# Kernel optimization log

Measured on AMD Instinct MI355X. Metric: run time of the kernel, lower is better.

## Reference

```python
import jax, jax.numpy as jnp
import numpy as np

B, T, C = 4, 2048, 2048
N_HEAD, N_KV = 16, 4
HD = C // N_HEAD          # 128
N_REP = N_HEAD // N_KV    # 4


def setup_inputs() -> dict:
    key = jax.random.key(0)
    k1, k2, k3 = jax.random.split(key, 3)
    x = jax.random.normal(k1, (B, T, C), dtype=jnp.float32)
    # RoPE frequencies: complex freqs_cis stored as [T, HD//2, 2] = (cos, sin)
    inv_freq = 1.0 / (10000.0 ** (jnp.arange(0, HD, 2, dtype=jnp.float32) / HD))  # [HD//2]
    angles = jnp.arange(T, dtype=jnp.float32)[:, None] * inv_freq[None, :]        # [T, HD//2]
    freqs_cis = jnp.stack([jnp.cos(angles), jnp.sin(angles)], axis=-1)            # [T, HD//2, 2]
    w_qkv = jax.random.normal(k2, (C, (N_HEAD + 2 * N_KV) * HD), dtype=jnp.float32) * 0.02
    w_proj = jax.random.normal(k3, (C, C), dtype=jnp.float32) * 0.02
    return {"x": x, "freqs_cis": freqs_cis, "w_qkv": w_qkv, "w_proj": w_proj}


def _apply_rope(t, freqs_cis):
    # t: [B, T, H, HD]; pairs (even, odd) along last dim form complex numbers
    shp = t.shape
    t2 = t.astype(jnp.float32).reshape(*shp[:-1], HD // 2, 2)
    cos = freqs_cis[None, :, None, :, 0]  # [1, T, 1, HD//2]
    sin = freqs_cis[None, :, None, :, 1]
    re = t2[..., 0] * cos - t2[..., 1] * sin
    im = t2[..., 0] * sin + t2[..., 1] * cos
    return jnp.stack([re, im], axis=-1).reshape(shp).astype(t.dtype)


def reference(x, freqs_cis, w_qkv, w_proj):
    Bs, Ts, Cs = x.shape
    qkv = x @ w_qkv  # [B, T, (H+2KV)*HD]
    q, k, v = jnp.split(qkv, [N_HEAD * HD, N_HEAD * HD + N_KV * HD], axis=-1)
    q = q.reshape(Bs, Ts, N_HEAD, HD)
    k = k.reshape(Bs, Ts, N_KV, HD)
    v = v.reshape(Bs, Ts, N_KV, HD)
    q = _apply_rope(q, freqs_cis)
    k = _apply_rope(k, freqs_cis)
    # GQA attention without materializing repeated k/v: group query heads per kv head
    qg = q.reshape(Bs, Ts, N_KV, N_REP, HD)
    scale = 1.0 / jnp.sqrt(jnp.asarray(HD, dtype=jnp.float32))
    scores = jnp.einsum('btkrd,bskd->bkrts', qg, k) * scale  # [B, KV, REP, T, T]
    att = jax.nn.softmax(scores.astype(jnp.float32), axis=-1).astype(q.dtype)
    y = jnp.einsum('bkrts,bskd->btkrd', att, v).reshape(Bs, Ts, Cs)
    return y @ w_proj
```

## Files before the change

### kernel.cpp

```cpp
#include <hip/hip_runtime.h>

using u16 = unsigned short;
using u32 = unsigned int;
typedef float f32x4 __attribute__((ext_vector_type(4)));
typedef float f32x16 __attribute__((ext_vector_type(16)));
typedef short s16x8 __attribute__((ext_vector_type(8)));
typedef unsigned int u32x4 __attribute__((ext_vector_type(4)));

__device__ __forceinline__ u16 f2bf(float x) {
  u32 u = __float_as_uint(x);
  u += 0x7fffu + ((u >> 16) & 1u);
  return (u16)(u >> 16);
}
__device__ __forceinline__ u32 pack2bf(float lo, float hi) {
  return (u32)f2bf(lo) | ((u32)f2bf(hi) << 16);
}
__device__ __forceinline__ float bf2f(u16 v) {
  return __uint_as_float(((u32)v) << 16);
}
__device__ __forceinline__ u32 cvtpk(float lo, float hi) {
  u32 r;
  asm("v_cvt_pk_bf16_f32 %0, %1, %2" : "=v"(r) : "v"(lo), "v"(hi));
  return r;
}
__device__ __forceinline__ void plswap(u32& a, u32& b) {
  asm volatile("v_permlane32_swap_b32 %0, %1" : "+v"(a), "+v"(b));
}
__device__ __forceinline__ void gload16(const u16* g, u16* l) {
  __builtin_amdgcn_global_load_lds(
      (__attribute__((address_space(1))) void*)(u16*)g,
      (__attribute__((address_space(3))) void*)l, 16, 0, 0);
}
__device__ __forceinline__ f32x4 fzero4() {
  f32x4 v = {0.f, 0.f, 0.f, 0.f};
  return v;
}
__device__ __forceinline__ f32x16 fzero16() {
  f32x16 v = {0, 0, 0, 0, 0, 0, 0, 0, 0, 0, 0, 0, 0, 0, 0, 0};
  return v;
}
__device__ __forceinline__ void barrier_hard() {
  __builtin_amdgcn_sched_barrier(0);
  __builtin_amdgcn_s_barrier();
  __builtin_amdgcn_sched_barrier(0);
}

__global__ __launch_bounds__(256) void k_convert(const float* __restrict__ in,
                                                 u16* __restrict__ out, int n8) {
  int i = blockIdx.x * 256 + threadIdx.x;
  if (i >= n8) return;
  const float4* p = (const float4*)in;
  float4 a = p[2 * i], b = p[2 * i + 1];
  uint4 o;
  o.x = pack2bf(a.x, a.y);
  o.y = pack2bf(a.z, a.w);
  o.z = pack2bf(b.x, b.y);
  o.w = pack2bf(b.z, b.w);
  ((uint4*)out)[i] = o;
}

__global__ __launch_bounds__(256) void k_transpose(const float* __restrict__ w,
                                                   u16* __restrict__ wt, int N, int K) {
  __shared__ float tile[64][65];
  int n0 = blockIdx.x * 64, k0 = blockIdx.y * 64;
  int tid = threadIdx.x;
  int rr = tid >> 6, cc = tid & 63;
#pragma unroll
  for (int p = 0; p < 16; ++p)
    tile[p * 4 + rr][cc] = w[(size_t)(k0 + p * 4 + rr) * N + n0 + cc];
  __syncthreads();
#pragma unroll
  for (int p = 0; p < 16; ++p)
    wt[(size_t)(n0 + p * 4 + rr) * K + k0 + cc] = f2bf(tile[cc][p * 4 + rr]);
}

template <bool OBF>
__global__ __launch_bounds__(512, 2) void k_gemm8(const u16* __restrict__ A,
                                                  const u16* __restrict__ Bt,
                                                  void* __restrict__ Out, int Nd, int Kd) {
  __shared__ u16 Al[2][2][8192];
  __shared__ u16 Bl[2][2][8192];
  u32 bid = blockIdx.x, nwg = gridDim.x;
  u32 wgid = (bid & 7) * (nwg >> 3) + (bid >> 3);
  int ntn = Nd >> 8;
  int bm = wgid / ntn, bn = wgid % ntn;
  int tid = threadIdx.x, w = tid >> 6, lane = tid & 63;
  int wm = w >> 2, wn = w & 3;
  int lq = lane & 15, lg = lane >> 4;

  const u16* Ab = A + (size_t)(bm * 256) * Kd;
  const u16* Bb = Bt + (size_t)(bn * 256) * Kd;

  u32 offA[2][2], offB[2][2];
#pragma unroll
  for (int set = 0; set < 2; ++set)
#pragma unroll
    for (int inst = 0; inst < 2; ++inst) {
      int c = inst * 512 + tid;
      int ldsrow = c >> 4, sl = c & 15;
      int orig = sl ^ (ldsrow & 15);
      int pr = ldsrow * 2 + (orig >> 3);
      int kch = orig & 7;
      int rA = (pr & 63) + ((pr >> 6) & 1) * 128 + set * 64;
      int rB = (pr & 31) + (pr >> 5) * 64 + set * 32;
      offA[set][inst] = (u32)(rA * Kd + kch * 8);
      offB[set][inst] = (u32)(rB * Kd + kch * 8);
    }

  int aoff[4][2], boff[4][2];
#pragma unroll
  for (int mf = 0; mf < 4; ++mf)
#pragma unroll
    for (int kk = 0; kk < 2; ++kk) {
      int pr = wm * 64 + mf * 16 + lq;
      int slot = (((pr & 1) << 3) + kk * 4 + lg) ^ ((pr >> 1) & 15);
      aoff[mf][kk] = (pr >> 1) * 128 + slot * 8;
    }
#pragma unroll
  for (int nf = 0; nf < 4; ++nf)
#pragma unroll
    for (int kk = 0; kk < 2; ++kk) {
      int pr = wn * 32 + (nf & 1) * 16 + lq;
      int slot = (((pr & 1) << 3) + kk * 4 + lg) ^ ((pr >> 1) & 15);
      boff[nf][kk] = (pr >> 1) * 128 + slot * 8;
    }

  int ldsbase = w * 512;

  auto stgA = [&](int dbuf, int set, int u) {
    const u16* s = Ab + u * 64;
    gload16(s + offA[set][0], &Al[dbuf][set][ldsbase]);
    gload16(s + offA[set][1], &Al[dbuf][set][4096 + ldsbase]);
  };
  auto stgB = [&](int dbuf, int set, int u) {
    const u16* s = Bb + u * 64;
    gload16(s + offB[set][0], &Bl[dbuf][set][ldsbase]);
    gload16(s + offB[set][1], &Bl[dbuf][set][4096 + ldsbase]);
  };

  f32x4 acc[8][4];
#pragma unroll
  for (int m = 0; m < 8; ++m)
#pragma unroll
    for (int n = 0; n < 4; ++n) acc[m][n] = fzero4();

  s16x8 af[4][2], bf[4][2];

  auto LDA = [&](int dbuf, int set) {
#pragma unroll
    for (int mf = 0; mf < 4; ++mf)
#pragma unroll
      for (int kk = 0; kk < 2; ++kk)
        af[mf][kk] = *(const s16x8*)&Al[dbuf][set][aoff[mf][kk]];
  };
  auto LDB = [&](int dbuf, int nf0) {
#pragma unroll
    for (int nf = 0; nf < 2; ++nf)
#pragma unroll
      for (int kk = 0; kk < 2; ++kk)
        bf[nf0 + nf][kk] = *(const s16x8*)&Bl[dbuf][nf0 >> 1][boff[nf0 + nf][kk]];
  };
  auto DO_MFMA = [&](int mb, int nb) {
    __builtin_amdgcn_s_setprio(1);
#pragma unroll
    for (int mf = 0; mf < 4; ++mf)
#pragma unroll
      for (int nf = 0; nf < 2; ++nf)
#pragma unroll
        for (int kk = 0; kk < 2; ++kk)
          acc[mb + mf][nb + nf] = __builtin_amdgcn_mfma_f32_16x16x32_bf16(
              af[mf][kk], bf[nb + nf][kk], acc[mb + mf][nb + nf], 0, 0, 0);
    __builtin_amdgcn_s_setprio(0);
  };
  auto LGKM0 = [&]() {
    asm volatile("s_waitcnt lgkmcnt(0)" ::: "memory");
    __builtin_amdgcn_sched_barrier(0);
  };

  int nt = Kd >> 6;
  stgA(0, 0, 0); stgB(0, 0, 0); stgA(0, 1, 0); stgB(0, 1, 0);
  stgA(1, 0, 1); stgB(1, 1, 1); stgA(1, 1, 1);
  asm volatile("s_waitcnt vmcnt(6)" ::: "memory");
  barrier_hard();

  for (int u = 0; u < nt; ++u) {
    int c = u & 1, nc = c ^ 1;
    bool g1 = (u + 1 < nt), g2 = (u + 2 < nt);
    LDA(c, 0);
    LDB(c, 0);
    if (g1) stgB(nc, 0, u + 1);
    barrier_hard();
    LGKM0();
    DO_MFMA(0, 0);
    barrier_hard();
    LDB(c, 2);
    if (g2) stgA(c, 0, u + 2);
    barrier_hard();
    LGKM0();
    DO_MFMA(0, 2);
    barrier_hard();
    LDA(c, 1);
    if (g2) stgB(c, 1, u + 2);
    barrier_hard();
    LGKM0();
    DO_MFMA(4, 2);
    barrier_hard();
    if (g2) stgA(c, 1, u + 2);
    barrier_hard();
    DO_MFMA(4, 0);
    if (g2) {
      asm volatile("s_waitcnt vmcnt(6)" ::: "memory");
    } else {
      asm volatile("s_waitcnt vmcnt(0)" ::: "memory");
    }
    barrier_hard();
  }

  int r0 = bm * 256 + wm * 128, c0 = bn * 256 + wn * 64;
  if (OBF) {
    u16* O = (u16*)Out;
#pragma unroll
    for (int mf = 0; mf < 8; ++mf)
#pragma unroll
      for (int nf = 0; nf < 4; ++nf)
#pragma unroll
        for (int r = 0; r < 4; ++r)
          O[(size_t)(r0 + mf * 16 + lg * 4 + r) * Nd + c0 + nf * 16 + lq] =
              f2bf(acc[mf][nf][r]);
  } else {
    float* O = (float*)Out;
#pragma unroll
    for (int mf = 0; mf < 8; ++mf)
#pragma unroll
      for (int nf = 0; nf < 4; ++nf)
#pragma unroll
        for (int r = 0; r < 4; ++r)
          O[(size_t)(r0 + mf * 16 + lg * 4 + r) * Nd + c0 + nf * 16 + lq] =
              acc[mf][nf][r];
  }
}

__device__ __forceinline__ u32 rope_pair(short a, short b, float c, float s, float sc) {
  float x0 = bf2f((u16)a), x1 = bf2f((u16)b);
  return pack2bf((x0 * c - x1 * s) * sc, (x0 * s + x1 * c) * sc);
}

__global__ __launch_bounds__(256) void k_ropeqk(const u16* __restrict__ qkv,
                                                const float* __restrict__ fr,
                                                u16* __restrict__ Q, u16* __restrict__ K) {
  int idx = blockIdx.x * 256 + threadIdx.x;
  if (idx >= 8192 * 320) return;
  int row = idx / 320, g = idx % 320;
  int b = row >> 11, t = row & 2047;
  int col = g * 8;
  const u16* src = qkv + (size_t)row * 3072 + col;
  int isq = col < 2048;
  float sc = isq ? 0.127517432f : 1.0f;
  int c2 = isq ? col : col - 2048;
  int h = c2 >> 7, d = c2 & 127;
  u16* dst = isq ? (Q + ((size_t)(b * 16 + h) * 2048 + t) * 128 + d)
                 : (K + ((size_t)(b * 4 + h) * 2048 + t) * 128 + d);
  const float4* fp = (const float4*)(fr + (size_t)t * 128 + d);
  float4 f01 = fp[0], f23 = fp[1];
  s16x8 v = *(const s16x8*)src;
  uint4 o;
  o.x = rope_pair(v[0], v[1], f01.x, f01.y, sc);
  o.y = rope_pair(v[2], v[3], f01.z, f01.w, sc);
  o.z = rope_pair(v[4], v[5], f23.x, f23.y, sc);
  o.w = rope_pair(v[6], v[7], f23.z, f23.w, sc);
  *(uint4*)dst = o;
}

__global__ __launch_bounds__(256) void k_vtrans(const u16* __restrict__ qkv,
                                                u16* __restrict__ Vt) {
  __shared__ u16 tile[128][68];
  int t0 = blockIdx.x * 64;
  int bh = blockIdx.y;
  int b = bh >> 2, h = bh & 3;
  int tid = threadIdx.x;
  const u16* src = qkv + ((size_t)(b * 2048 + t0)) * 3072 + 2560 + h * 128;
#pragma unroll
  for (int i = 0; i < 4; ++i) {
    int c = tid + 256 * i;
    int r = c >> 4, col = c & 15;
    uint4 v = *(const uint4*)(src + (size_t)r * 3072 + col * 8);
    u16 e[8];
    *(uint4*)e = v;
#pragma unroll
    for (int j = 0; j < 8; ++j) tile[col * 8 + j][r] = e[j];
  }
  __syncthreads();
  u16* dst = Vt + ((size_t)bh * 128) * 2048 + t0;
#pragma unroll
  for (int i = 0; i < 4; ++i) {
    int c = tid + 256 * i;
    int d = c >> 3, part = c & 7;
    uint2 lo = *(const uint2*)&tile[d][part * 8];
    uint2 hi = *(const uint2*)&tile[d][part * 8 + 4];
    uint4 o = make_uint4(lo.x, lo.y, hi.x, hi.y);
    *(uint4*)&dst[(size_t)d * 2048 + part * 8] = o;
  }
}

__global__ __launch_bounds__(256, 2) void k_attn(const u16* __restrict__ Qg,
                                                 const u16* __restrict__ Kg,
                                                 const u16* __restrict__ Vg,
                                                 u16* __restrict__ Yg) {
  __shared__ u16 Kl[2][64 * 128];
  __shared__ u16 Vl[2][64 * 128];
  u32 bid = blockIdx.x;
  u32 wgid = (bid & 7) * 128 + (bid >> 3);
  int qt = wgid & 15, bh = wgid >> 4;
  int b = bh >> 4, h = bh & 15, kvh = h >> 2;
  int tid = threadIdx.x, w = tid >> 6, lane = tid & 63;
  int l31 = lane & 31, hi = lane >> 5;
  const u16* Qb = Qg + ((size_t)bh * 2048 + qt * 128 + w * 32 + l31) * 128;
  const u16* Kb = Kg + (size_t)(b * 4 + kvh) * 2048 * 128;
  const u16* Vb = Vg + (size_t)(b * 4 + kvh) * 128 * 2048;

  s16x8 qf[8];
#pragma unroll
  for (int kc = 0; kc < 8; ++kc)
    qf[kc] = *(const s16x8*)(Qb + kc * 16 + hi * 8);

  f32x16 o[4];
#pragma unroll
  for (int i = 0; i < 4; ++i) o[i] = fzero16();
  float l_run = 0.f;

  int krow4 = lane >> 4;
  int kc_ = lane & 15;
  u32 offV[4];
#pragma unroll
  for (int i = 0; i < 4; ++i) {
    int c = i * 256 + tid;
    int ldsrow = c >> 4, sl = c & 15;
    int orig = sl ^ (ldsrow & 15);
    int d = ldsrow * 2 + (orig >> 3);
    int kch = orig & 7;
    offV[i] = (u32)(d * 2048 + kch * 8);
  }

  auto stageK = [&](int buf, int key0) {
#pragma unroll
    for (int i = 0; i < 4; ++i) {
      int key = w * 16 + i * 4 + krow4;
      gload16(Kb + (size_t)(key0 + key) * 128 + ((kc_ ^ (key & 15)) * 8),
              &Kl[buf][(w * 16 + i * 4) * 128]);
    }
  };
  auto stageV = [&](int buf, int key0) {
#pragma unroll
    for (int i = 0; i < 4; ++i)
      gload16(Vb + key0 + offV[i], &Vl[buf][(i * 256 + w * 64) * 8]);
  };

  stageK(0, 0);
  stageV(0, 0);
  __syncthreads();

  for (int kt = 0; kt < 32; ++kt) {
    int cur = kt & 1;
    if (kt < 31) {
      stageK(cur ^ 1, (kt + 1) * 64);
      stageV(cur ^ 1, (kt + 1) * 64);
    }

    f32x16 s0 = fzero16(), s1 = fzero16();
    int swz = l31 & 15;
    __builtin_amdgcn_s_setprio(1);
#pragma unroll
    for (int kc = 0; kc < 8; ++kc) {
      int slot = (kc * 2 + hi) ^ swz;
      s16x8 a0 = *(const s16x8*)&Kl[cur][l31 * 128 + slot * 8];
      s0 = __builtin_amdgcn_mfma_f32_32x32x16_bf16(a0, qf[kc], s0, 0, 0, 0);
      s16x8 a1 = *(const s16x8*)&Kl[cur][(32 + l31) * 128 + slot * 8];
      s1 = __builtin_amdgcn_mfma_f32_32x32x16_bf16(a1, qf[kc], s1, 0, 0, 0);
    }
    __builtin_amdgcn_s_setprio(0);

    u32 pw[16];
    float ps = 0.f;
    auto sm_half = [&](const f32x16& sv, u32* pwg) {
#pragma unroll
      for (int g = 0; g < 2; ++g) {
        float p[8];
#pragma unroll
        for (int j = 0; j < 8; ++j) p[j] = exp2f(sv[g * 8 + j]);
        ps += ((p[0] + p[1]) + (p[2] + p[3])) + ((p[4] + p[5]) + (p[6] + p[7]));
        u32 x0 = cvtpk(p[0], p[1]), y0 = cvtpk(p[4], p[5]);
        u32 x1 = cvtpk(p[2], p[3]), y1 = cvtpk(p[6], p[7]);
        plswap(x0, y0);
        plswap(x1, y1);
        pwg[g * 4 + 0] = x0;
        pwg[g * 4 + 1] = x1;
        pwg[g * 4 + 2] = y0;
        pwg[g * 4 + 3] = y1;
      }
    };
    sm_half(s0, pw);
    sm_half(s1, pw + 8);
    l_run += ps;

    __builtin_amdgcn_s_setprio(1);
#pragma unroll
    for (int g = 0; g < 4; ++g) {
      u32x4 t;
      t.x = pw[g * 4 + 0];
      t.y = pw[g * 4 + 1];
      t.z = pw[g * 4 + 2];
      t.w = pw[g * 4 + 3];
      s16x8 pf = __builtin_bit_cast(s16x8, t);
#pragma unroll
      for (int df = 0; df < 4; ++df) {
        int d = df * 32 + l31;
        int slot = (((d & 1) << 3) + g * 2 + hi) ^ ((d >> 1) & 15);
        s16x8 vf = *(const s16x8*)&Vl[cur][(d >> 1) * 128 + slot * 8];
        o[df] = __builtin_amdgcn_mfma_f32_32x32x16_bf16(vf, pf, o[df], 0, 0, 0);
      }
    }
    __builtin_amdgcn_s_setprio(0);

    __syncthreads();
  }

  l_run += __shfl_xor(l_run, 32);
  float inv = 1.0f / l_run;
  int q = qt * 128 + w * 32 + l31;
  u16* yr = Yg + ((size_t)(b * 2048) + q) * 2048 + h * 128;
#pragma unroll
  for (int df = 0; df < 4; ++df)
#pragma unroll
    for (int q4 = 0; q4 < 4; ++q4) {
      int d0 = df * 32 + q4 * 8 + hi * 4;
      uint2 vv;
      vv.x = cvtpk(o[df][q4 * 4 + 0] * inv, o[df][q4 * 4 + 1] * inv);
      vv.y = cvtpk(o[df][q4 * 4 + 2] * inv, o[df][q4 * 4 + 3] * inv);
      *(uint2*)&yr[d0] = vv;
    }
}

extern "C" void kernel_launch(void* const* d_in, const int* in_sizes, int n_in,
                              void* d_out, int out_size, void* d_ws, size_t ws_size,
                              hipStream_t stream) {
  const float* x = (const float*)d_in[0];
  const float* fr = (const float*)d_in[1];
  const float* wqkv = (const float*)d_in[2];
  const float* wproj = (const float*)d_in[3];
  char* ws = (char*)d_ws;
  u16* xbf = (u16*)(ws + 0);
  u16* wqkvT = (u16*)(ws + 33554432);
  u16* wprojT = (u16*)(ws + 46137344);
  u16* qkv = (u16*)(ws + 54525952);
  u16* Qb = (u16*)(ws + 104857600);
  u16* Kb = (u16*)(ws + 138412032);
  u16* Vtb = (u16*)(ws + 146800640);

  k_convert<<<8192, 256, 0, stream>>>(x, xbf, 8192 * 2048 / 8);
  k_transpose<<<dim3(48, 32), 256, 0, stream>>>(wqkv, wqkvT, 3072, 2048);
  k_transpose<<<dim3(32, 32), 256, 0, stream>>>(wproj, wprojT, 2048, 2048);
  k_gemm8<true><<<32 * 12, 512, 0, stream>>>(xbf, wqkvT, qkv, 3072, 2048);
  k_ropeqk<<<10240, 256, 0, stream>>>(qkv, fr, Qb, Kb);
  k_vtrans<<<dim3(32, 16), 256, 0, stream>>>(qkv, Vtb);
  k_attn<<<1024, 256, 0, stream>>>(Qb, Kb, Vtb, xbf);
  k_gemm8<false><<<32 * 8, 512, 0, stream>>>(xbf, wprojT, d_out, 2048, 2048);
}
```

Measured before the change: 397.3 us.

## Software-pipeline QK^T of next tile with softmax/PV in attention, merge prep launches

Restructures the attention loop so the QK^T MFMAs for the next key tile run interleaved with the exp/PV work of the current tile. K is prefetched two tiles ahead and V one tile ahead, so matrix-core work overlaps softmax VALU work. It also merges the convert and two transpose kernels into one launch, and the rope and V-transpose kernels into another, to cut launch overhead. In exchange it holds more accumulator registers live, which may raise register pressure or cause spills under the 2-wave occupancy bound.

```diff
diff --git a/kernel.cpp b/kernel.cpp
--- a/kernel.cpp
+++ b/kernel.cpp
@@ -45,25 +45,40 @@
   __builtin_amdgcn_sched_barrier(0);
 }
 
-__global__ __launch_bounds__(256) void k_convert(const float* __restrict__ in,
-                                                 u16* __restrict__ out, int n8) {
-  int i = blockIdx.x * 256 + threadIdx.x;
-  if (i >= n8) return;
-  const float4* p = (const float4*)in;
-  float4 a = p[2 * i], b = p[2 * i + 1];
-  uint4 o;
-  o.x = pack2bf(a.x, a.y);
-  o.y = pack2bf(a.z, a.w);
-  o.z = pack2bf(b.x, b.y);
-  o.w = pack2bf(b.z, b.w);
-  ((uint4*)out)[i] = o;
-}
-
-__global__ __launch_bounds__(256) void k_transpose(const float* __restrict__ w,
-                                                   u16* __restrict__ wt, int N, int K) {
+__global__ __launch_bounds__(256) void k_prep(const float* __restrict__ x,
+                                              u16* __restrict__ xbf,
+                                              const float* __restrict__ wqkv,
+                                              u16* __restrict__ wqkvT,
+                                              const float* __restrict__ wproj,
+                                              u16* __restrict__ wprojT) {
+  int bid = blockIdx.x, tid = threadIdx.x;
+  if (bid < 8192) {
+    int i = bid * 256 + tid;
+    const float4* p = (const float4*)x;
+    float4 a = p[2 * i], b = p[2 * i + 1];
+    uint4 o;
+    o.x = pack2bf(a.x, a.y);
+    o.y = pack2bf(a.z, a.w);
+    o.z = pack2bf(b.x, b.y);
+    o.w = pack2bf(b.z, b.w);
+    ((uint4*)xbf)[i] = o;
+    return;
+  }
   __shared__ float tile[64][65];
-  int n0 = blockIdx.x * 64, k0 = blockIdx.y * 64;
-  int tid = threadIdx.x;
+  int N, K, n0, k0;
+  const float* w;
+  u16* wt;
+  if (bid < 9728) {
+    int t = bid - 8192;
+    n0 = (t % 48) * 64;
+    k0 = (t / 48) * 64;
+    w = wqkv; wt = wqkvT; N = 3072; K = 2048;
+  } else {
+    int t = bid - 9728;
+    n0 = (t % 32) * 64;
+    k0 = (t / 32) * 64;
+    w = wproj; wt = wprojT; N = 2048; K = 2048;
+  }
   int rr = tid >> 6, cc = tid & 63;
 #pragma unroll
   for (int p = 0; p < 16; ++p)
@@ -245,39 +260,38 @@
   return pack2bf((x0 * c - x1 * s) * sc, (x0 * s + x1 * c) * sc);
 }
 
-__global__ __launch_bounds__(256) void k_ropeqk(const u16* __restrict__ qkv,
-                                                const float* __restrict__ fr,
-                                                u16* __restrict__ Q, u16* __restrict__ K) {
-  int idx = blockIdx.x * 256 + threadIdx.x;
-  if (idx >= 8192 * 320) return;
-  int row = idx / 320, g = idx % 320;
-  int b = row >> 11, t = row & 2047;
-  int col = g * 8;
-  const u16* src = qkv + (size_t)row * 3072 + col;
-  int isq = col < 2048;
-  float sc = isq ? 0.127517432f : 1.0f;
-  int c2 = isq ? col : col - 2048;
-  int h = c2 >> 7, d = c2 & 127;
-  u16* dst = isq ? (Q + ((size_t)(b * 16 + h) * 2048 + t) * 128 + d)
-                 : (K + ((size_t)(b * 4 + h) * 2048 + t) * 128 + d);
-  const float4* fp = (const float4*)(fr + (size_t)t * 128 + d);
-  float4 f01 = fp[0], f23 = fp[1];
-  s16x8 v = *(const s16x8*)src;
-  uint4 o;
-  o.x = rope_pair(v[0], v[1], f01.x, f01.y, sc);
-  o.y = rope_pair(v[2], v[3], f01.z, f01.w, sc);
-  o.z = rope_pair(v[4], v[5], f23.x, f23.y, sc);
-  o.w = rope_pair(v[6], v[7], f23.z, f23.w, sc);
-  *(uint4*)dst = o;
-}
-
-__global__ __launch_bounds__(256) void k_vtrans(const u16* __restrict__ qkv,
-                                                u16* __restrict__ Vt) {
+__global__ __launch_bounds__(256) void k_rope_all(const u16* __restrict__ qkv,
+                                                  const float* __restrict__ fr,
+                                                  u16* __restrict__ Q, u16* __restrict__ K,
+                                                  u16* __restrict__ Vt) {
+  int bid = blockIdx.x, tid = threadIdx.x;
+  if (bid < 10240) {
+    int idx = bid * 256 + tid;
+    int row = idx / 320, g = idx % 320;
+    int b = row >> 11, t = row & 2047;
+    int col = g * 8;
+    const u16* src = qkv + (size_t)row * 3072 + col;
+    int isq = col < 2048;
+    float sc = isq ? 0.127517432f : 1.0f;
+    int c2 = isq ? col : col - 2048;
+    int h = c2 >> 7, d = c2 & 127;
+    u16* dst = isq ? (Q + ((size_t)(b * 16 + h) * 2048 + t) * 128 + d)
+                   : (K + ((size_t)(b * 4 + h) * 2048 + t) * 128 + d);
+    const float4* fp = (const float4*)(fr + (size_t)t * 128 + d);
+    float4 f01 = fp[0], f23 = fp[1];
+    s16x8 v = *(const s16x8*)src;
+    uint4 o;
+    o.x = rope_pair(v[0], v[1], f01.x, f01.y, sc);
+    o.y = rope_pair(v[2], v[3], f01.z, f01.w, sc);
+    o.z = rope_pair(v[4], v[5], f23.x, f23.y, sc);
+    o.w = rope_pair(v[6], v[7], f23.z, f23.w, sc);
+    *(uint4*)dst = o;
+    return;
+  }
   __shared__ u16 tile[128][68];
-  int t0 = blockIdx.x * 64;
-  int bh = blockIdx.y;
+  int vb = bid - 10240;
+  int t0 = (vb & 31) * 64, bh = vb >> 5;
   int b = bh >> 2, h = bh & 3;
-  int tid = threadIdx.x;
   const u16* src = qkv + ((size_t)(b * 2048 + t0)) * 3072 + 2560 + h * 128;
 #pragma unroll
   for (int i = 0; i < 4; ++i) {
@@ -296,8 +310,8 @@
     int c = tid + 256 * i;
     int d = c >> 3, part = c & 7;
     uint2 lo = *(const uint2*)&tile[d][part * 8];
-    uint2 hi = *(const uint2*)&tile[d][part * 8 + 4];
-    uint4 o = make_uint4(lo.x, lo.y, hi.x, hi.y);
+    uint2 hi2 = *(const uint2*)&tile[d][part * 8 + 4];
+    uint4 o = make_uint4(lo.x, lo.y, hi2.x, hi2.y);
     *(uint4*)&dst[(size_t)d * 2048 + part * 8] = o;
   }
 }
@@ -355,73 +369,70 @@
       gload16(Vb + key0 + offV[i], &Vl[buf][(i * 256 + w * 64) * 8]);
   };
 
+  int swz = l31 & 15;
+  auto qk2 = [&](int buf, int g, f32x16& n0, f32x16& n1) {
+#pragma unroll
+    for (int kc = 2 * g; kc <= 2 * g + 1; ++kc) {
+      int slot = (kc * 2 + hi) ^ swz;
+      s16x8 a0 = *(const s16x8*)&Kl[buf][l31 * 128 + slot * 8];
+      n0 = __builtin_amdgcn_mfma_f32_32x32x16_bf16(a0, qf[kc], n0, 0, 0, 0);
+      s16x8 a1 = *(const s16x8*)&Kl[buf][(32 + l31) * 128 + slot * 8];
+      n1 = __builtin_amdgcn_mfma_f32_32x32x16_bf16(a1, qf[kc], n1, 0, 0, 0);
+    }
+  };
+
   stageK(0, 0);
   stageV(0, 0);
+  stageK(1, 64);
   __syncthreads();
-
-  for (int kt = 0; kt < 32; ++kt) {
-    int cur = kt & 1;
-    if (kt < 31) {
-      stageK(cur ^ 1, (kt + 1) * 64);
-      stageV(cur ^ 1, (kt + 1) * 64);
-    }
-
-    f32x16 s0 = fzero16(), s1 = fzero16();
-    int swz = l31 & 15;
-    __builtin_amdgcn_s_setprio(1);
-#pragma unroll
-    for (int kc = 0; kc < 8; ++kc) {
-      int slot = (kc * 2 + hi) ^ swz;
-      s16x8 a0 = *(const s16x8*)&Kl[cur][l31 * 128 + slot * 8];
-      s0 = __builtin_amdgcn_mfma_f32_32x32x16_bf16(a0, qf[kc], s0, 0, 0, 0);
-      s16x8 a1 = *(const s16x8*)&Kl[cur][(32 + l31) * 128 + slot * 8];
-      s1 = __builtin_amdgcn_mfma_f32_32x32x16_bf16(a1, qf[kc], s1, 0, 0, 0);
-    }
-    __builtin_amdgcn_s_setprio(0);
-
-    u32 pw[16];
-    float ps = 0.f;
-    auto sm_half = [&](const f32x16& sv, u32* pwg) {
-#pragma unroll
-      for (int g = 0; g < 2; ++g) {
-        float p[8];
-#pragma unroll
-        for (int j = 0; j < 8; ++j) p[j] = exp2f(sv[g * 8 + j]);
-        ps += ((p[0] + p[1]) + (p[2] + p[3])) + ((p[4] + p[5]) + (p[6] + p[7]));
-        u32 x0 = cvtpk(p[0], p[1]), y0 = cvtpk(p[4], p[5]);
-        u32 x1 = cvtpk(p[2], p[3]), y1 = cvtpk(p[6], p[7]);
-        plswap(x0, y0);
-        plswap(x1, y1);
-        pwg[g * 4 + 0] = x0;
-        pwg[g * 4 + 1] = x1;
-        pwg[g * 4 + 2] = y0;
-        pwg[g * 4 + 3] = y1;
-      }
-    };
-    sm_half(s0, pw);
-    sm_half(s1, pw + 8);
-    l_run += ps;
-
-    __builtin_amdgcn_s_setprio(1);
+  f32x16 cA0 = fzero16(), cA1 = fzero16(), cB0 = fzero16(), cB1 = fzero16();
+#pragma unroll
+  for (int g = 0; g < 4; ++g) qk2(0, g, cA0, cA1);
+  __syncthreads();
+
+  auto body = [&](int t, f32x16& c0, f32x16& c1, f32x16& n0, f32x16& n1) {
+    bool hasN = (t + 1 < 32), hasK2 = (t + 2 < 32);
+    if (hasN) stageV((t + 1) & 1, (t + 1) * 64);
+    if (hasK2) stageK(t & 1, (t + 2) * 64);
+    if (hasN) {
+      n0 = fzero16();
+      n1 = fzero16();
+    }
+    int kbuf = (t + 1) & 1, vbuf = t & 1;
 #pragma unroll
     for (int g = 0; g < 4; ++g) {
-      u32x4 t;
-      t.x = pw[g * 4 + 0];
-      t.y = pw[g * 4 + 1];
-      t.z = pw[g * 4 + 2];
-      t.w = pw[g * 4 + 3];
-      s16x8 pf = __builtin_bit_cast(s16x8, t);
+      __builtin_amdgcn_s_setprio(1);
+      if (hasN) qk2(kbuf, g, n0, n1);
+      __builtin_amdgcn_s_setprio(0);
+      const f32x16& sv = (g < 2) ? c0 : c1;
+      int g2 = g & 1;
+      float p[8];
+#pragma unroll
+      for (int j = 0; j < 8; ++j) p[j] = exp2f(sv[g2 * 8 + j]);
+      l_run += ((p[0] + p[1]) + (p[2] + p[3])) + ((p[4] + p[5]) + (p[6] + p[7]));
+      u32 x0 = cvtpk(p[0], p[1]), y0 = cvtpk(p[4], p[5]);
+      u32 x1 = cvtpk(p[2], p[3]), y1 = cvtpk(p[6], p[7]);
+      plswap(x0, y0);
+      plswap(x1, y1);
+      u32x4 tw;
+      tw.x = x0; tw.y = x1; tw.z = y0; tw.w = y1;
+      s16x8 pf = __builtin_bit_cast(s16x8, tw);
+      __builtin_amdgcn_s_setprio(1);
 #pragma unroll
       for (int df = 0; df < 4; ++df) {
         int d = df * 32 + l31;
         int slot = (((d & 1) << 3) + g * 2 + hi) ^ ((d >> 1) & 15);
-        s16x8 vf = *(const s16x8*)&Vl[cur][(d >> 1) * 128 + slot * 8];
+        s16x8 vf = *(const s16x8*)&Vl[vbuf][(d >> 1) * 128 + slot * 8];
         o[df] = __builtin_amdgcn_mfma_f32_32x32x16_bf16(vf, pf, o[df], 0, 0, 0);
       }
-    }
-    __builtin_amdgcn_s_setprio(0);
-
+      __builtin_amdgcn_s_setprio(0);
+    }
     __syncthreads();
+  };
+
+  for (int t = 0; t < 32; t += 2) {
+    body(t, cA0, cA1, cB0, cB1);
+    body(t + 1, cB0, cB1, cA0, cA1);
   }
 
   l_run += __shfl_xor(l_run, 32);
@@ -456,12 +467,9 @@
   u16* Kb = (u16*)(ws + 138412032);
   u16* Vtb = (u16*)(ws + 146800640);
 
-  k_convert<<<8192, 256, 0, stream>>>(x, xbf, 8192 * 2048 / 8);
-  k_transpose<<<dim3(48, 32), 256, 0, stream>>>(wqkv, wqkvT, 3072, 2048);
-  k_transpose<<<dim3(32, 32), 256, 0, stream>>>(wproj, wprojT, 2048, 2048);
+  k_prep<<<10752, 256, 0, stream>>>(x, xbf, wqkv, wqkvT, wproj, wprojT);
   k_gemm8<true><<<32 * 12, 512, 0, stream>>>(xbf, wqkvT, qkv, 3072, 2048);
-  k_ropeqk<<<10240, 256, 0, stream>>>(qkv, fr, Qb, Kb);
-  k_vtrans<<<dim3(32, 16), 256, 0, stream>>>(qkv, Vtb);
+  k_rope_all<<<10752, 256, 0, stream>>>(qkv, fr, Qb, Kb, Vtb);
   k_attn<<<1024, 256, 0, stream>>>(Qb, Kb, Vtb, xbf);
   k_gemm8<false><<<32 * 8, 512, 0, stream>>>(xbf, wprojT, d_out, 2048, 2048);
 }
```

Measured after the change: 395.8 us. About the same (-0.4%).
